# Kernel tuning notes

Hardware: AMD Instinct MI355X
Metric: run time of the kernel (lower is better)

## Reference

```python
import jax, jax.numpy as jnp
import numpy as np

D_MODEL = 1024
NUM_HEADS = 16
D_K = D_MODEL // NUM_HEADS
THETA = 10000.0
MAX_SEQ_LEN = 2048
BATCH = 2
SEQ = 2048


def setup_inputs() -> dict:
    key = jax.random.key(0)
    ks = jax.random.split(key, 5)
    std = np.sqrt(2.0 / (D_MODEL + D_MODEL)).astype(np.float32)
    x = jax.random.normal(ks[0], (BATCH, SEQ, D_MODEL), dtype=jnp.float32)
    Wq = jax.random.normal(ks[1], (D_MODEL, D_MODEL), dtype=jnp.float32) * std
    Wk = jax.random.normal(ks[2], (D_MODEL, D_MODEL), dtype=jnp.float32) * std
    Wv = jax.random.normal(ks[3], (D_MODEL, D_MODEL), dtype=jnp.float32) * std
    Wo = jax.random.normal(ks[4], (D_MODEL, D_MODEL), dtype=jnp.float32) * std
    token_positions = jnp.arange(SEQ, dtype=jnp.int32)
    return {"x": x, "token_positions": token_positions,
            "Wq": Wq, "Wk": Wk, "Wv": Wv, "Wo": Wo}


def _rope_tables(positions):
    # freqs: [d_k/2]; angles: [seq, d_k/2]
    freqs = 1.0 / (THETA ** (jnp.arange(0, D_K, 2, dtype=jnp.float32) / D_K))
    angles = positions.astype(jnp.float32)[:, None] * freqs[None, :]
    return jnp.cos(angles), jnp.sin(angles)


def _apply_rope(t, cos, sin):
    # t: [b, h, s, d_k]; cos/sin: [s, d_k/2]; interleaved pair rotation
    x1 = t[..., 0::2]
    x2 = t[..., 1::2]
    r1 = x1 * cos - x2 * sin
    r2 = x1 * sin + x2 * cos
    return jnp.stack([r1, r2], axis=-1).reshape(t.shape)


def reference(x, token_positions, Wq, Wk, Wv, Wo):
    b, s, _ = x.shape
    # projections: y = x W^T
    q = jnp.einsum('bsi,oi->bso', x, Wq)
    k = jnp.einsum('bsi,oi->bso', x, Wk)
    v = jnp.einsum('bsi,oi->bso', x, Wv)
    # split heads: [b, h, s, d]
    q = q.reshape(b, s, NUM_HEADS, D_K).transpose(0, 2, 1, 3)
    k = k.reshape(b, s, NUM_HEADS, D_K).transpose(0, 2, 1, 3)
    v = v.reshape(b, s, NUM_HEADS, D_K).transpose(0, 2, 1, 3)
    cos, sin = _rope_tables(token_positions)
    q = _apply_rope(q, cos, sin)
    k = _apply_rope(k, cos, sin)
    scale = jnp.asarray(D_K, jnp.float32) ** 0.5
    scores = jnp.einsum('bhqd,bhkd->bhqk', q, k) / scale
    causal = jnp.tril(jnp.ones((s, s), dtype=bool))
    scores = jnp.where(causal, scores, -jnp.inf)
    attn = jax.nn.softmax(scores.astype(jnp.float32), axis=-1).astype(scores.dtype)
    out = jnp.einsum('bhqk,bhkd->bhqd', attn, v)
    out = out.transpose(0, 2, 1, 3).reshape(b, s, D_MODEL)
    return jnp.einsum('bsi,oi->bso', out, Wo)
```

## Files before the change

kernel.cpp:

```cpp
#include <hip/hip_runtime.h>
#include <stdint.h>

#define D_MODEL 1024
#define NH      16
#define DKH     64
#define SEQLEN  2048
#define BATCH   2
#define KDIM    1024

typedef __attribute__((ext_vector_type(8))) short          short8;
typedef __attribute__((ext_vector_type(8))) unsigned short ushort8;
typedef __attribute__((ext_vector_type(4))) float          f32x4;

__device__ __forceinline__ unsigned short f2bf(float f) {
    union { float f; unsigned u; } v; v.f = f;
    unsigned u = v.u;
    unsigned r = (u + 0x7FFFu + ((u >> 16) & 1u)) >> 16;
    return (unsigned short)r;
}
__device__ __forceinline__ float bf2f(unsigned short h) {
    union { unsigned u; float f; } v; v.u = ((unsigned)h) << 16;
    return v.f;
}

__device__ __forceinline__ void gload_lds16(const unsigned short* g, unsigned short* l) {
    __builtin_amdgcn_global_load_lds(
        (__attribute__((address_space(1))) void*)(g),
        (__attribute__((address_space(3))) void*)(l), 16, 0, 0);
}

__global__ void cvt_kernel(const float* __restrict__ src, unsigned short* __restrict__ dst) {
    int i = (blockIdx.x * 256 + threadIdx.x) * 8;
    float4 a = *(const float4*)(src + i);
    float4 b = *(const float4*)(src + i + 4);
    ushort8 o;
    o[0] = f2bf(a.x); o[1] = f2bf(a.y); o[2] = f2bf(a.z); o[3] = f2bf(a.w);
    o[4] = f2bf(b.x); o[5] = f2bf(b.y); o[6] = f2bf(b.z); o[7] = f2bf(b.w);
    *(ushort8*)(dst + i) = o;
}

__device__ __forceinline__ void gemm_core_128(
    const unsigned short* __restrict__ A, const unsigned short* __restrict__ W,
    unsigned short* a_lds, unsigned short* b_lds,
    int m0, int n0, f32x4 acc[4][4])
{
    const int tid  = threadIdx.x;
    const int lane = tid & 63;
    const int w    = tid >> 6;
    const int quad = lane >> 4;
    const int l16  = lane & 15;
    const int wm   = w & 1, wn = w >> 1;

    const int srow = lane >> 2;
    const int scol = (lane & 3) * 8;

    #pragma unroll
    for (int mi = 0; mi < 4; mi++)
        #pragma unroll
        for (int ni = 0; ni < 4; ni++) {
            f32x4 z = {0.f, 0.f, 0.f, 0.f};
            acc[mi][ni] = z;
        }

    for (int kk = 0; kk < KDIM; kk += 32) {
        __syncthreads();
        #pragma unroll
        for (int i = 0; i < 2; ++i) {
            int c = 2 * w + i;
            gload_lds16(A + (size_t)(m0 + c * 16 + srow) * KDIM + kk + scol, &a_lds[c * 512]);
            gload_lds16(W + (size_t)(n0 + c * 16 + srow) * KDIM + kk + scol, &b_lds[c * 512]);
        }
        __syncthreads();

        short8 af[4], bf[4];
        #pragma unroll
        for (int i = 0; i < 4; i++) {
            af[i] = *(const short8*)&a_lds[(wm * 64 + i * 16 + l16) * 32 + quad * 8];
            bf[i] = *(const short8*)&b_lds[(wn * 64 + i * 16 + l16) * 32 + quad * 8];
        }
        #pragma unroll
        for (int mi = 0; mi < 4; mi++)
            #pragma unroll
            for (int ni = 0; ni < 4; ni++)
                acc[mi][ni] = __builtin_amdgcn_mfma_f32_16x16x32_bf16(af[mi], bf[ni], acc[mi][ni], 0, 0, 0);
    }
}

__global__ __launch_bounds__(256, 2)
void gemm_qkv(const unsigned short* __restrict__ X,
              const unsigned short* __restrict__ Wq,
              const unsigned short* __restrict__ Wk,
              const unsigned short* __restrict__ Wv,
              unsigned short* __restrict__ q_ws,
              unsigned short* __restrict__ k_ws,
              unsigned short* __restrict__ v_ws)
{
    __shared__ __align__(16) unsigned short a_lds[128 * 32];
    __shared__ __align__(16) unsigned short b_lds[128 * 32];

    const int z = blockIdx.z;
    const unsigned short* W = (z == 0) ? Wq : ((z == 1) ? Wk : Wv);
    const int m0 = blockIdx.x * 128, n0 = blockIdx.y * 128;

    f32x4 acc[4][4];
    gemm_core_128(X, W, a_lds, b_lds, m0, n0, acc);

    const int lane = threadIdx.x & 63;
    const int w    = threadIdx.x >> 6;
    const int quad = lane >> 4;
    const int l16  = lane & 15;
    const int wm   = w & 1, wn = w >> 1;

    #pragma unroll
    for (int mi = 0; mi < 4; mi++)
        #pragma unroll
        for (int ni = 0; ni < 4; ni++)
            #pragma unroll
            for (int r = 0; r < 4; r++) {
                int row = m0 + wm * 64 + mi * 16 + quad * 4 + r;
                int col = n0 + wn * 64 + ni * 16 + l16;
                int b = row >> 11, s = row & 2047;
                int h = col >> 6,  d = col & 63;
                int bh = b * NH + h;
                float val = acc[mi][ni][r];
                if (z == 2) {
                    v_ws[(size_t)bh * DKH * SEQLEN + (size_t)d * SEQLEN + s] = f2bf(val);
                } else {
                    unsigned short* dst = (z == 0) ? q_ws : k_ws;
                    dst[(size_t)bh * SEQLEN * DKH + (size_t)s * DKH + d] = f2bf(val);
                }
            }
}

__global__ void rope_kernel(const int* __restrict__ pos,
                            unsigned short* __restrict__ q_ws,
                            unsigned short* __restrict__ k_ws)
{
    int i = blockIdx.x * 256 + threadIdx.x;
    unsigned short* t = (i >> 19) ? k_ws : q_ws;
    int c   = i & 0x7FFFF;
    int bh  = c >> 14;
    int rem = c & 16383;
    int s   = rem >> 3;
    int ch  = rem & 7;
    size_t base = (size_t)bh * (SEQLEN * DKH) + (size_t)s * DKH + ch * 8;

    ushort8 v = *(ushort8*)(t + base);
    float p = (float)pos[s];
    ushort8 o;
    #pragma unroll
    for (int u = 0; u < 4; u++) {
        int j = ch * 4 + u;
        float freq = expf(-((float)(2 * j) * (1.0f / 64.0f)) * 9.210340371976184f);
        float ang = p * freq;
        float sn, cn;
        sincosf(ang, &sn, &cn);
        float x1 = bf2f(v[2 * u]);
        float x2 = bf2f(v[2 * u + 1]);
        o[2 * u]     = f2bf(x1 * cn - x2 * sn);
        o[2 * u + 1] = f2bf(x1 * sn + x2 * cn);
    }
    *(ushort8*)(t + base) = o;
}

__global__ __launch_bounds__(256, 2)
void attn_kernel(const unsigned short* __restrict__ q_ws,
                 const unsigned short* __restrict__ k_ws,
                 const unsigned short* __restrict__ v_ws,
                 unsigned short* __restrict__ ao)
{
    __shared__ __align__(16) unsigned short k_lds[64 * 72];
    __shared__ __align__(16) unsigned short v_lds[64 * 72];
    __shared__ __align__(16) unsigned short p_lds[4 * 16 * 72];

    const int p   = blockIdx.x;
    const int bh  = blockIdx.y;
    const int tid = threadIdx.x, lane = tid & 63, w = tid >> 6;
    const int quad = lane >> 4, l16 = lane & 15;

    const size_t kqbase = (size_t)bh * SEQLEN * DKH;
    const size_t vbase  = (size_t)bh * DKH * SEQLEN;
    const int b = bh >> 4, h = bh & 15;

    const int row0 = tid >> 3;
    const int c0   = (tid & 7) * 8;

    #pragma unroll
    for (int phase = 0; phase < 2; ++phase) {
        const int qt  = (phase == 0) ? (31 - p) : p;
        const int q0  = qt * 64;
        const int qw0 = q0 + w * 16;

        short8 aq[2];
        #pragma unroll
        for (int kc = 0; kc < 2; kc++)
            aq[kc] = *(const short8*)(q_ws + kqbase + (size_t)(qw0 + l16) * DKH + kc * 32 + quad * 8);

        f32x4 o_acc[4];
        #pragma unroll
        for (int df = 0; df < 4; df++) { f32x4 z = {0.f,0.f,0.f,0.f}; o_acc[df] = z; }
        float l_i[4] = {0.f, 0.f, 0.f, 0.f};

        ushort8 kreg[2], vreg[2];
        #pragma unroll
        for (int rr = 0; rr < 2; ++rr) {
            int row = row0 + rr * 32;
            kreg[rr] = *(const ushort8*)(k_ws + kqbase + (size_t)row * DKH + c0);
            vreg[rr] = *(const ushort8*)(v_ws + vbase + (size_t)row * SEQLEN + c0);
        }

        for (int t = 0; t <= qt; ++t) {
            const int s0 = t * 64;
            __syncthreads();
            #pragma unroll
            for (int rr = 0; rr < 2; ++rr) {
                int row = row0 + rr * 32;
                *(ushort8*)&k_lds[row * 72 + c0] = kreg[rr];
                *(ushort8*)&v_lds[row * 72 + c0] = vreg[rr];
            }
            __syncthreads();
            if (t < qt) {
                int s1 = s0 + 64;
                #pragma unroll
                for (int rr = 0; rr < 2; ++rr) {
                    int row = row0 + rr * 32;
                    kreg[rr] = *(const ushort8*)(k_ws + kqbase + (size_t)(s1 + row) * DKH + c0);
                    vreg[rr] = *(const ushort8*)(v_ws + vbase + (size_t)row * SEQLEN + s1 + c0);
                }
            }

            f32x4 sf[4];
            #pragma unroll
            for (int nf = 0; nf < 4; nf++) {
                f32x4 s = {0.f,0.f,0.f,0.f};
                #pragma unroll
                for (int kc = 0; kc < 2; kc++) {
                    short8 bk = *(const short8*)&k_lds[(nf * 16 + l16) * 72 + kc * 32 + quad * 8];
                    s = __builtin_amdgcn_mfma_f32_16x16x32_bf16(aq[kc], bk, s, 0, 0, 0);
                }
                sf[nf] = s;
            }

            if (t == qt) {
                #pragma unroll
                for (int nf = 0; nf < 4; nf++)
                    #pragma unroll
                    for (int r = 0; r < 4; r++) {
                        int qg = qw0 + quad * 4 + r;
                        int kg = s0 + nf * 16 + l16;
                        float pv = (kg <= qg) ? __expf(sf[nf][r] * 0.125f) : 0.f;
                        sf[nf][r] = pv;
                        l_i[r] += pv;
                    }
            } else {
                #pragma unroll
                for (int nf = 0; nf < 4; nf++)
                    #pragma unroll
                    for (int r = 0; r < 4; r++) {
                        float pv = __expf(sf[nf][r] * 0.125f);
                        sf[nf][r] = pv;
                        l_i[r] += pv;
                    }
            }

            #pragma unroll
            for (int nf = 0; nf < 4; nf++)
                #pragma unroll
                for (int r = 0; r < 4; r++)
                    p_lds[w * 1152 + (quad * 4 + r) * 72 + nf * 16 + l16] = f2bf(sf[nf][r]);

            short8 ap[2];
            #pragma unroll
            for (int kc = 0; kc < 2; kc++)
                ap[kc] = *(const short8*)&p_lds[w * 1152 + l16 * 72 + kc * 32 + quad * 8];
            #pragma unroll
            for (int df = 0; df < 4; df++)
                #pragma unroll
                for (int kc = 0; kc < 2; kc++) {
                    short8 bv = *(const short8*)&v_lds[(df * 16 + l16) * 72 + kc * 32 + quad * 8];
                    o_acc[df] = __builtin_amdgcn_mfma_f32_16x16x32_bf16(ap[kc], bv, o_acc[df], 0, 0, 0);
                }
        }

        #pragma unroll
        for (int r = 0; r < 4; r++) {
            float rs = l_i[r];
            rs += __shfl_xor(rs, 1);
            rs += __shfl_xor(rs, 2);
            rs += __shfl_xor(rs, 4);
            rs += __shfl_xor(rs, 8);
            float inv = 1.0f / rs;
            int qg = qw0 + quad * 4 + r;
            #pragma unroll
            for (int df = 0; df < 4; df++)
                ao[(size_t)(b * SEQLEN + qg) * D_MODEL + h * DKH + df * 16 + l16] =
                    f2bf(o_acc[df][r] * inv);
        }
    }
}

__global__ __launch_bounds__(256, 2)
void gemm_out(const unsigned short* __restrict__ AO,
              const unsigned short* __restrict__ Wo,
              float* __restrict__ out)
{
    __shared__ __align__(16) unsigned short a_lds[128 * 32];
    __shared__ __align__(16) unsigned short b_lds[128 * 32];

    const int m0 = blockIdx.x * 128, n0 = blockIdx.y * 128;
    f32x4 acc[4][4];
    gemm_core_128(AO, Wo, a_lds, b_lds, m0, n0, acc);

    const int lane = threadIdx.x & 63;
    const int w    = threadIdx.x >> 6;
    const int quad = lane >> 4;
    const int l16  = lane & 15;
    const int wm   = w & 1, wn = w >> 1;

    #pragma unroll
    for (int mi = 0; mi < 4; mi++)
        #pragma unroll
        for (int ni = 0; ni < 4; ni++)
            #pragma unroll
            for (int r = 0; r < 4; r++) {
                int row = m0 + wm * 64 + mi * 16 + quad * 4 + r;
                int col = n0 + wn * 64 + ni * 16 + l16;
                out[(size_t)row * D_MODEL + col] = acc[mi][ni][r];
            }
}

extern "C" void kernel_launch(void* const* d_in, const int* in_sizes, int n_in,
                              void* d_out, int out_size, void* d_ws, size_t ws_size,
                              hipStream_t stream) {
    const float* X  = (const float*)d_in[0];
    const int*   pos = (const int*)d_in[1];
    const float* Wq = (const float*)d_in[2];
    const float* Wk = (const float*)d_in[3];
    const float* Wv = (const float*)d_in[4];
    const float* Wo = (const float*)d_in[5];
    float* out = (float*)d_out;

    unsigned short* Xb  = (unsigned short*)d_ws;
    unsigned short* Wqb = Xb + 4194304;
    unsigned short* Wkb = Wqb + 1048576;
    unsigned short* Wvb = Wkb + 1048576;
    unsigned short* Wob = Wvb + 1048576;
    unsigned short* q_ws = Wob + 1048576;
    unsigned short* k_ws = q_ws + 4194304;
    unsigned short* v_ws = k_ws + 4194304;
    unsigned short* ao   = v_ws + 4194304;

    cvt_kernel<<<dim3(2048), dim3(256), 0, stream>>>(X,  Xb);
    cvt_kernel<<<dim3(512),  dim3(256), 0, stream>>>(Wq, Wqb);
    cvt_kernel<<<dim3(512),  dim3(256), 0, stream>>>(Wk, Wkb);
    cvt_kernel<<<dim3(512),  dim3(256), 0, stream>>>(Wv, Wvb);
    cvt_kernel<<<dim3(512),  dim3(256), 0, stream>>>(Wo, Wob);

    gemm_qkv<<<dim3(32, 8, 3), dim3(256), 0, stream>>>(Xb, Wqb, Wkb, Wvb, q_ws, k_ws, v_ws);
    rope_kernel<<<dim3(4096), dim3(256), 0, stream>>>(pos, q_ws, k_ws);
    attn_kernel<<<dim3(16, 32), dim3(256), 0, stream>>>(q_ws, k_ws, v_ws, ao);
    gemm_out<<<dim3(32, 8), dim3(256), 0, stream>>>(ao, Wob, out);
}
```

Measured before the change: 201.4 us.

## Widen attention KV tile to 128, merge conversion launches, reorder attention grid

The attention kernel now processes 128 keys per iteration instead of 64, which halves the number of barrier-synchronised loop trips and doubles the MFMA work between syncs. For odd query tiles the last 128-key chunk is partly masked, so some extra work is done. The five fp32-to-bf16 conversion launches are merged into one 2D launch that exits early for out-of-range blocks. The attention grid is swapped to (bh, p) so neighbouring blocks handle different heads. The larger tile raises LDS use and register pressure, which may lower occupancy.

After: 196.2 us. 1.03x faster.

```diff
diff --git a/kernel.cpp b/kernel.cpp
--- a/kernel.cpp
+++ b/kernel.cpp
@@ -29,8 +29,21 @@
         (__attribute__((address_space(3))) void*)(l), 16, 0, 0);
 }
 
-__global__ void cvt_kernel(const float* __restrict__ src, unsigned short* __restrict__ dst) {
+__global__ void cvt_all(const float* __restrict__ X,  const float* __restrict__ Wq,
+                        const float* __restrict__ Wk, const float* __restrict__ Wv,
+                        const float* __restrict__ Wo,
+                        unsigned short* __restrict__ Xb,  unsigned short* __restrict__ Wqb,
+                        unsigned short* __restrict__ Wkb, unsigned short* __restrict__ Wvb,
+                        unsigned short* __restrict__ Wob) {
+    const int z = blockIdx.y;
+    const float* src; unsigned short* dst; int n;
+    if (z == 0)      { src = X;  dst = Xb;  n = 4194304; }
+    else if (z == 1) { src = Wq; dst = Wqb; n = 1048576; }
+    else if (z == 2) { src = Wk; dst = Wkb; n = 1048576; }
+    else if (z == 3) { src = Wv; dst = Wvb; n = 1048576; }
+    else             { src = Wo; dst = Wob; n = 1048576; }
     int i = (blockIdx.x * 256 + threadIdx.x) * 8;
+    if (i >= n) return;
     float4 a = *(const float4*)(src + i);
     float4 b = *(const float4*)(src + i + 4);
     ushort8 o;
@@ -169,12 +182,12 @@
                  const unsigned short* __restrict__ v_ws,
                  unsigned short* __restrict__ ao)
 {
-    __shared__ __align__(16) unsigned short k_lds[64 * 72];
-    __shared__ __align__(16) unsigned short v_lds[64 * 72];
-    __shared__ __align__(16) unsigned short p_lds[4 * 16 * 72];
-
-    const int p   = blockIdx.x;
-    const int bh  = blockIdx.y;
+    __shared__ __align__(16) unsigned short k_lds[128 * 72];
+    __shared__ __align__(16) unsigned short v_lds[64 * 136];
+    __shared__ __align__(16) unsigned short p_lds[4 * 16 * 136];
+
+    const int bh  = blockIdx.x;
+    const int p   = blockIdx.y;
     const int tid = threadIdx.x, lane = tid & 63, w = tid >> 6;
     const int quad = lane >> 4, l16 = lane & 15;
 
@@ -182,14 +195,15 @@
     const size_t vbase  = (size_t)bh * DKH * SEQLEN;
     const int b = bh >> 4, h = bh & 15;
 
-    const int row0 = tid >> 3;
-    const int c0   = (tid & 7) * 8;
+    const int krow = tid >> 3, kcol = (tid & 7) * 8;
+    const int vrow = tid >> 4, vcol = (tid & 15) * 8;
 
     #pragma unroll
     for (int phase = 0; phase < 2; ++phase) {
         const int qt  = (phase == 0) ? (31 - p) : p;
         const int q0  = qt * 64;
         const int qw0 = q0 + w * 16;
+        const int nt  = (qt + 2) >> 1;
 
         short8 aq[2];
         #pragma unroll
@@ -201,37 +215,34 @@
         for (int df = 0; df < 4; df++) { f32x4 z = {0.f,0.f,0.f,0.f}; o_acc[df] = z; }
         float l_i[4] = {0.f, 0.f, 0.f, 0.f};
 
-        ushort8 kreg[2], vreg[2];
-        #pragma unroll
-        for (int rr = 0; rr < 2; ++rr) {
-            int row = row0 + rr * 32;
-            kreg[rr] = *(const ushort8*)(k_ws + kqbase + (size_t)row * DKH + c0);
-            vreg[rr] = *(const ushort8*)(v_ws + vbase + (size_t)row * SEQLEN + c0);
-        }
-
-        for (int t = 0; t <= qt; ++t) {
-            const int s0 = t * 64;
+        ushort8 kreg[4], vreg[4];
+        #pragma unroll
+        for (int rr = 0; rr < 4; ++rr) {
+            kreg[rr] = *(const ushort8*)(k_ws + kqbase + (size_t)(krow + rr * 32) * DKH + kcol);
+            vreg[rr] = *(const ushort8*)(v_ws + vbase + (size_t)(vrow + rr * 16) * SEQLEN + vcol);
+        }
+
+        for (int t = 0; t < nt; ++t) {
+            const int s0 = t * 128;
             __syncthreads();
             #pragma unroll
-            for (int rr = 0; rr < 2; ++rr) {
-                int row = row0 + rr * 32;
-                *(ushort8*)&k_lds[row * 72 + c0] = kreg[rr];
-                *(ushort8*)&v_lds[row * 72 + c0] = vreg[rr];
+            for (int rr = 0; rr < 4; ++rr) {
+                *(ushort8*)&k_lds[(krow + rr * 32) * 72 + kcol]  = kreg[rr];
+                *(ushort8*)&v_lds[(vrow + rr * 16) * 136 + vcol] = vreg[rr];
             }
             __syncthreads();
-            if (t < qt) {
-                int s1 = s0 + 64;
-                #pragma unroll
-                for (int rr = 0; rr < 2; ++rr) {
-                    int row = row0 + rr * 32;
-                    kreg[rr] = *(const ushort8*)(k_ws + kqbase + (size_t)(s1 + row) * DKH + c0);
-                    vreg[rr] = *(const ushort8*)(v_ws + vbase + (size_t)row * SEQLEN + s1 + c0);
+            if (t < nt - 1) {
+                int s1 = s0 + 128;
+                #pragma unroll
+                for (int rr = 0; rr < 4; ++rr) {
+                    kreg[rr] = *(const ushort8*)(k_ws + kqbase + (size_t)(s1 + krow + rr * 32) * DKH + kcol);
+                    vreg[rr] = *(const ushort8*)(v_ws + vbase + (size_t)(vrow + rr * 16) * SEQLEN + s1 + vcol);
                 }
             }
 
-            f32x4 sf[4];
-            #pragma unroll
-            for (int nf = 0; nf < 4; nf++) {
+            f32x4 sf[8];
+            #pragma unroll
+            for (int nf = 0; nf < 8; nf++) {
                 f32x4 s = {0.f,0.f,0.f,0.f};
                 #pragma unroll
                 for (int kc = 0; kc < 2; kc++) {
@@ -241,9 +252,9 @@
                 sf[nf] = s;
             }
 
-            if (t == qt) {
-                #pragma unroll
-                for (int nf = 0; nf < 4; nf++)
+            if (t == nt - 1) {
+                #pragma unroll
+                for (int nf = 0; nf < 8; nf++)
                     #pragma unroll
                     for (int r = 0; r < 4; r++) {
                         int qg = qw0 + quad * 4 + r;
@@ -254,7 +265,7 @@
                     }
             } else {
                 #pragma unroll
-                for (int nf = 0; nf < 4; nf++)
+                for (int nf = 0; nf < 8; nf++)
                     #pragma unroll
                     for (int r = 0; r < 4; r++) {
                         float pv = __expf(sf[nf][r] * 0.125f);
@@ -264,20 +275,20 @@
             }
 
             #pragma unroll
-            for (int nf = 0; nf < 4; nf++)
+            for (int nf = 0; nf < 8; nf++)
                 #pragma unroll
                 for (int r = 0; r < 4; r++)
-                    p_lds[w * 1152 + (quad * 4 + r) * 72 + nf * 16 + l16] = f2bf(sf[nf][r]);
-
-            short8 ap[2];
-            #pragma unroll
-            for (int kc = 0; kc < 2; kc++)
-                ap[kc] = *(const short8*)&p_lds[w * 1152 + l16 * 72 + kc * 32 + quad * 8];
+                    p_lds[w * 2176 + (quad * 4 + r) * 136 + nf * 16 + l16] = f2bf(sf[nf][r]);
+
+            short8 ap[4];
+            #pragma unroll
+            for (int kc = 0; kc < 4; kc++)
+                ap[kc] = *(const short8*)&p_lds[w * 2176 + l16 * 136 + kc * 32 + quad * 8];
             #pragma unroll
             for (int df = 0; df < 4; df++)
                 #pragma unroll
-                for (int kc = 0; kc < 2; kc++) {
-                    short8 bv = *(const short8*)&v_lds[(df * 16 + l16) * 72 + kc * 32 + quad * 8];
+                for (int kc = 0; kc < 4; kc++) {
+                    short8 bv = *(const short8*)&v_lds[(df * 16 + l16) * 136 + kc * 32 + quad * 8];
                     o_acc[df] = __builtin_amdgcn_mfma_f32_16x16x32_bf16(ap[kc], bv, o_acc[df], 0, 0, 0);
                 }
         }
@@ -350,14 +361,10 @@
     unsigned short* v_ws = k_ws + 4194304;
     unsigned short* ao   = v_ws + 4194304;
 
-    cvt_kernel<<<dim3(2048), dim3(256), 0, stream>>>(X,  Xb);
-    cvt_kernel<<<dim3(512),  dim3(256), 0, stream>>>(Wq, Wqb);
-    cvt_kernel<<<dim3(512),  dim3(256), 0, stream>>>(Wk, Wkb);
-    cvt_kernel<<<dim3(512),  dim3(256), 0, stream>>>(Wv, Wvb);
-    cvt_kernel<<<dim3(512),  dim3(256), 0, stream>>>(Wo, Wob);
-
+    cvt_all<<<dim3(2048, 5), dim3(256), 0, stream>>>(X, Wq, Wk, Wv, Wo,
+                                                     Xb, Wqb, Wkb, Wvb, Wob);
     gemm_qkv<<<dim3(32, 8, 3), dim3(256), 0, stream>>>(Xb, Wqb, Wkb, Wvb, q_ws, k_ws, v_ws);
     rope_kernel<<<dim3(4096), dim3(256), 0, stream>>>(pos, q_ws, k_ws);
-    attn_kernel<<<dim3(16, 32), dim3(256), 0, stream>>>(q_ws, k_ws, v_ws, ao);
+    attn_kernel<<<dim3(32, 16), dim3(256), 0, stream>>>(q_ws, k_ws, v_ws, ao);
     gemm_out<<<dim3(32, 8), dim3(256), 0, stream>>>(ao, Wob, out);
 }
```
